# Performance work log

Measured on AMD Instinct MI355X. Metric: run time of the kernel, lower is better.

## Reference

```python
import jax, jax.numpy as jnp
import numpy as np

QMAX = 127.0  # int8 symmetric range used by quanto absmax quantizer


def setup_inputs() -> dict:
    key = jax.random.key(0)
    k1, k2, k3 = jax.random.split(key, 3)
    x = jax.random.normal(k1, (4, 2048, 1600), dtype=jnp.float32)
    weight = jax.random.normal(k2, (1600, 6400), dtype=jnp.float32) * 0.02  # Conv1D init std=0.02
    bias = jax.random.normal(k3, (6400,), dtype=jnp.float32) * 0.02
    in_scale = jnp.float32(0.02)   # calibration scale for activations
    out_scale = jnp.float32(0.05)  # calibration scale for outputs
    return {"x": x, "weight": weight, "bias": bias, "in_scale": in_scale, "out_scale": out_scale}


def reference(x, weight, bias, in_scale, out_scale):
    # --- quantize input to int8 with the fixed in_scale (QTensor.quantize) ---
    x_q = jnp.clip(jnp.round(x / in_scale), -128, 127).astype(jnp.int32)
    # --- quantize weight to int8 with absmax scale (QTensor.quantize default) ---
    w_scale = jnp.max(jnp.abs(weight)) / QMAX
    w_q = jnp.clip(jnp.round(weight / w_scale), -128, 127).astype(jnp.int32)
    # --- quantize bias to int32 at the accumulator scale ---
    bias_scale = in_scale * w_scale
    b_q = jnp.round(bias / bias_scale).astype(jnp.int32)
    # --- int32-accumulated addmm: [B*S, nx] @ [nx, nf] + [nf] ---
    bsz = x.shape[:-1]
    nx = x.shape[-1]
    acc_i32 = jnp.matmul(x_q.reshape(-1, nx), w_q,
                         preferred_element_type=jnp.int32) + b_q[None, :]
    # --- rescale int32 accumulator (scale=bias_scale) to int8 at out_scale ---
    out_q = jnp.clip(jnp.round(acc_i32.astype(jnp.float32) * (bias_scale / out_scale)),
                     -128, 127).astype(jnp.int8)
    # return the dequantized value the downstream layer would see
    out = out_q.astype(jnp.float32) * out_scale
    return out.reshape(*bsz, -1)
```

## Files before the change

kernel.cpp:

```cpp
#include <hip/hip_runtime.h>


#define M_DIM 8192
#define K_DIM 1600
#define N_DIM 6400
#define QMAXF 127.0f

typedef __attribute__((ext_vector_type(4))) int int4v;


__device__ __forceinline__ void load_lds16(const void* gptr, void* lptr) {
    __builtin_amdgcn_global_load_lds((__attribute__((address_space(1))) void*)gptr,
                                     (__attribute__((address_space(3))) void*)lptr,
                                     16, 0, 0);
}

__global__ void wmax_kernel(const float* __restrict__ w,
                            unsigned int* __restrict__ wmax_bits, int n4) {
    __shared__ float smax[4];
    const float4* w4 = (const float4*)w;
    int i = blockIdx.x * blockDim.x + threadIdx.x;
    int stride = gridDim.x * blockDim.x;
    float m = 0.0f;
    for (; i < n4; i += stride) {
        float4 v = w4[i];
        m = fmaxf(m, fmaxf(fmaxf(fabsf(v.x), fabsf(v.y)),
                           fmaxf(fabsf(v.z), fabsf(v.w))));
    }
#pragma unroll
    for (int off = 32; off > 0; off >>= 1)
        m = fmaxf(m, __shfl_down(m, off, 64));
    const int wave = threadIdx.x >> 6;
    if ((threadIdx.x & 63) == 0) smax[wave] = m;
    __syncthreads();
    if (threadIdx.x == 0) {
        float mm = fmaxf(fmaxf(smax[0], smax[1]), fmaxf(smax[2], smax[3]));
        atomicMax(wmax_bits, __float_as_uint(mm));
    }
}

__global__ void quantx_kernel(const float* __restrict__ x, signed char* __restrict__ xq,
                              const float* __restrict__ in_scale_p, int n4) {
    int i = blockIdx.x * blockDim.x + threadIdx.x;
    if (i >= n4) return;
    float s = *in_scale_p;
    float4 v = ((const float4*)x)[i];
    float a = fminf(fmaxf(rintf(v.x / s), -128.0f), 127.0f);
    float b = fminf(fmaxf(rintf(v.y / s), -128.0f), 127.0f);
    float c = fminf(fmaxf(rintf(v.z / s), -128.0f), 127.0f);
    float d = fminf(fmaxf(rintf(v.w / s), -128.0f), 127.0f);
    char4 packed = make_char4((signed char)a, (signed char)b,
                              (signed char)c, (signed char)d);
    ((char4*)xq)[i] = packed;
}

__global__ void quantw_kernel(const float* __restrict__ w, signed char* __restrict__ wT,
                              const unsigned int* __restrict__ wmax_bits) {
    __shared__ signed char tile[64 * 80];
    const float wscale = __uint_as_float(*wmax_bits) / QMAXF;
    const int n0 = blockIdx.x * 64;
    const int k0 = blockIdx.y * 64;
    const int tid = threadIdx.x;
    const int nn = tid & 63;
    const int kb = tid >> 6;
#pragma unroll
    for (int p = 0; p < 16; ++p) {
        const int kk = p * 4 + kb;
        float v = w[(size_t)(k0 + kk) * N_DIM + n0 + nn];
        float q = fminf(fmaxf(rintf(v / wscale), -128.0f), 127.0f);
        tile[nn * 80 + kk] = (signed char)q;
    }
    __syncthreads();
    const int n_loc = tid >> 2;
    const int kq = tid & 3;
    int4v val = *(const int4v*)&tile[n_loc * 80 + kq * 16];
    *(int4v*)&wT[(size_t)(n0 + n_loc) * K_DIM + k0 + kq * 16] = val;
}

__global__ __launch_bounds__(256, 2) void gemm_i8_kernel(
        const signed char* __restrict__ xq, const signed char* __restrict__ wTq,
        const float* __restrict__ bias, const unsigned int* __restrict__ wmax_bits,
        const float* __restrict__ in_scale_p, const float* __restrict__ out_scale_p,
        float* __restrict__ out) {
    __shared__ signed char A_lds[2][128 * 64];
    __shared__ signed char B_lds[2][128 * 64];

    const int tid   = threadIdx.x;
    const int wave  = tid >> 6;
    const int lane  = tid & 63;
    const int quad  = lane >> 4;
    const int l15   = lane & 15;
    const int waveM = wave >> 1;
    const int waveN = wave & 1;

    const int gid   = blockIdx.x;
    const int xcd   = gid & 7;
    const int idx   = gid >> 3;
    const int n_blk = idx >> 3;
    const int m_blk = (xcd << 3) | (idx & 7);

    const int blockN0 = n_blk * 128;
    const int blockM0 = m_blk * 128;

    const signed char* Ag = xq  + (size_t)blockM0 * K_DIM;
    const signed char* Bg = wTq + (size_t)blockN0 * K_DIM;

    const int srow = wave * 16 + (lane >> 2);
    const int scol = (((lane & 3) ^ ((lane >> 3) & 3)) * 16);

    int4v acc[4][4];
    const int4v zero4 = {0, 0, 0, 0};
#pragma unroll
    for (int i = 0; i < 4; ++i)
#pragma unroll
        for (int j = 0; j < 4; ++j) acc[i][j] = zero4;

#pragma unroll
    for (int t = 0; t < 2; ++t) {
        const int r = t * 64 + srow;
        load_lds16(Ag + (size_t)r * K_DIM + scol, &A_lds[0][(t * 64 + wave * 16) * 64]);
        load_lds16(Bg + (size_t)r * K_DIM + scol, &B_lds[0][(t * 64 + wave * 16) * 64]);
    }

    const int rchunk = (quad ^ ((l15 >> 1) & 3)) * 16;

    int buf = 0;
    for (int kn = 64; kn <= K_DIM; kn += 64) {
        __syncthreads();

        if (kn < K_DIM) {
            const int nb = buf ^ 1;
#pragma unroll
            for (int t = 0; t < 2; ++t) {
                const int r = t * 64 + srow;
                load_lds16(Ag + (size_t)r * K_DIM + kn + scol,
                           &A_lds[nb][(t * 64 + wave * 16) * 64]);
                load_lds16(Bg + (size_t)r * K_DIM + kn + scol,
                           &B_lds[nb][(t * 64 + wave * 16) * 64]);
            }
        }

        int4v a[4], b[4];
#pragma unroll
        for (int mt = 0; mt < 4; ++mt)
            a[mt] = *(const int4v*)&A_lds[buf][(waveM * 64 + mt * 16 + l15) * 64 + rchunk];
#pragma unroll
        for (int nt = 0; nt < 4; ++nt)
            b[nt] = *(const int4v*)&B_lds[buf][(waveN * 64 + nt * 16 + l15) * 64 + rchunk];

#pragma unroll
        for (int mt = 0; mt < 4; ++mt)
#pragma unroll
            for (int nt = 0; nt < 4; ++nt)
                acc[mt][nt] = __builtin_amdgcn_mfma_i32_16x16x64_i8(a[mt], b[nt],
                                                                    acc[mt][nt], 0, 0, 0);
        buf ^= 1;
    }

    const float s_in  = *in_scale_p;
    const float s_out = *out_scale_p;
    const float wscale = __uint_as_float(*wmax_bits) / QMAXF;
    const float bias_scale = s_in * wscale;
    const float ratio = bias_scale / s_out;

#pragma unroll
    for (int nt = 0; nt < 4; ++nt) {
        const int col = blockN0 + waveN * 64 + nt * 16 + l15;
        const int bq = (int)rintf(bias[col] / bias_scale);
#pragma unroll
        for (int mt = 0; mt < 4; ++mt) {
#pragma unroll
            for (int r = 0; r < 4; ++r) {
                const int row = blockM0 + waveM * 64 + mt * 16 + quad * 4 + r;
                const int av = acc[mt][nt][r] + bq;
                float f = rintf((float)av * ratio);
                f = fminf(fmaxf(f, -128.0f), 127.0f);
                out[(size_t)row * N_DIM + col] = f * s_out;
            }
        }
    }
}

extern "C" void kernel_launch(void* const* d_in, const int* in_sizes, int n_in,
                              void* d_out, int out_size, void* d_ws, size_t ws_size,
                              hipStream_t stream) {
    const float* x         = (const float*)d_in[0];
    const float* w         = (const float*)d_in[1];
    const float* bias      = (const float*)d_in[2];
    const float* in_scale  = (const float*)d_in[3];
    const float* out_scale = (const float*)d_in[4];
    float* out = (float*)d_out;

    unsigned char* ws = (unsigned char*)d_ws;
    unsigned int* wmax_bits = (unsigned int*)ws;
    signed char* xq  = (signed char*)(ws + 256);
    signed char* wTq = (signed char*)(ws + 256 + (size_t)M_DIM * K_DIM);

    hipMemsetAsync(d_ws, 0, 256, stream);

    wmax_kernel<<<320, 256, 0, stream>>>(w, wmax_bits, (K_DIM * N_DIM) / 4);

    quantx_kernel<<<(M_DIM * K_DIM / 4 + 255) / 256, 256, 0, stream>>>(
        x, xq, in_scale, M_DIM * K_DIM / 4);

    dim3 wgrid(N_DIM / 64, K_DIM / 64);
    quantw_kernel<<<wgrid, 256, 0, stream>>>(w, wTq, wmax_bits);

    gemm_i8_kernel<<<3200, 256, 0, stream>>>(xq, wTq, bias, wmax_bits,
                                             in_scale, out_scale, out);
}
```

Baseline: 434.9 us.

## Triple-buffer LDS in int8 GEMM with explicit vmcnt waits

Turns the GEMM main loop from double to triple buffering. Global-to-LDS loads run two k-tiles ahead, and fine-grained s_waitcnt vmcnt counts replace the full __syncthreads, so more load latency can overlap with MFMA work. LDS use grows from 32KB to 48KB per block, which may affect the occupancy target of 2 blocks per CU. The hand-written wait counts also depend on the exact number of outstanding loads per stage.

```diff
diff --git a/kernel.cpp b/kernel.cpp
--- a/kernel.cpp
+++ b/kernel.cpp
@@ -82,8 +82,8 @@
         const float* __restrict__ bias, const unsigned int* __restrict__ wmax_bits,
         const float* __restrict__ in_scale_p, const float* __restrict__ out_scale_p,
         float* __restrict__ out) {
-    __shared__ signed char A_lds[2][128 * 64];
-    __shared__ signed char B_lds[2][128 * 64];
+    __shared__ signed char A_lds[3][128 * 64];
+    __shared__ signed char B_lds[3][128 * 64];
 
     const int tid   = threadIdx.x;
     const int wave  = tid >> 6;
@@ -115,47 +115,65 @@
 #pragma unroll
         for (int j = 0; j < 4; ++j) acc[i][j] = zero4;
 
-#pragma unroll
-    for (int t = 0; t < 2; ++t) {
-        const int r = t * 64 + srow;
-        load_lds16(Ag + (size_t)r * K_DIM + scol, &A_lds[0][(t * 64 + wave * 16) * 64]);
-        load_lds16(Bg + (size_t)r * K_DIM + scol, &B_lds[0][(t * 64 + wave * 16) * 64]);
-    }
-
     const int rchunk = (quad ^ ((l15 >> 1) & 3)) * 16;
 
-    int buf = 0;
-    for (int kn = 64; kn <= K_DIM; kn += 64) {
-        __syncthreads();
-
-        if (kn < K_DIM) {
-            const int nb = buf ^ 1;
-#pragma unroll
-            for (int t = 0; t < 2; ++t) {
-                const int r = t * 64 + srow;
-                load_lds16(Ag + (size_t)r * K_DIM + kn + scol,
-                           &A_lds[nb][(t * 64 + wave * 16) * 64]);
-                load_lds16(Bg + (size_t)r * K_DIM + kn + scol,
-                           &B_lds[nb][(t * 64 + wave * 16) * 64]);
-            }
+    const int NT = K_DIM / 64;
+
+    auto STAGE = [&](int sb, int kt) {
+        const int kof = kt * 64;
+#pragma unroll
+        for (int t = 0; t < 2; ++t) {
+            const int r = t * 64 + srow;
+            load_lds16(Ag + (size_t)r * K_DIM + kof + scol,
+                       &A_lds[sb][(t * 64 + wave * 16) * 64]);
+            load_lds16(Bg + (size_t)r * K_DIM + kof + scol,
+                       &B_lds[sb][(t * 64 + wave * 16) * 64]);
         }
-
+    };
+
+    auto COMPUTE = [&](int cb) {
         int4v a[4], b[4];
 #pragma unroll
         for (int mt = 0; mt < 4; ++mt)
-            a[mt] = *(const int4v*)&A_lds[buf][(waveM * 64 + mt * 16 + l15) * 64 + rchunk];
+            a[mt] = *(const int4v*)&A_lds[cb][(waveM * 64 + mt * 16 + l15) * 64 + rchunk];
 #pragma unroll
         for (int nt = 0; nt < 4; ++nt)
-            b[nt] = *(const int4v*)&B_lds[buf][(waveN * 64 + nt * 16 + l15) * 64 + rchunk];
-
+            b[nt] = *(const int4v*)&B_lds[cb][(waveN * 64 + nt * 16 + l15) * 64 + rchunk];
 #pragma unroll
         for (int mt = 0; mt < 4; ++mt)
 #pragma unroll
             for (int nt = 0; nt < 4; ++nt)
                 acc[mt][nt] = __builtin_amdgcn_mfma_i32_16x16x64_i8(a[mt], b[nt],
                                                                     acc[mt][nt], 0, 0, 0);
-        buf ^= 1;
-    }
+    };
+
+    STAGE(0, 0);
+    STAGE(1, 1);
+
+    int cb = 0;
+    for (int t = 0; t < NT - 2; ++t) {
+        const int sb = (cb == 0) ? 2 : cb - 1;
+        STAGE(sb, t + 2);
+        asm volatile("s_waitcnt vmcnt(8)" ::: "memory");
+        __builtin_amdgcn_s_barrier();
+        __builtin_amdgcn_sched_barrier(0);
+        COMPUTE(cb);
+        asm volatile("s_waitcnt lgkmcnt(0)" ::: "memory");
+        __builtin_amdgcn_sched_barrier(0);
+        __builtin_amdgcn_s_barrier();
+        cb = (cb == 2) ? 0 : cb + 1;
+    }
+
+    asm volatile("s_waitcnt vmcnt(4)" ::: "memory");
+    __builtin_amdgcn_s_barrier();
+    __builtin_amdgcn_sched_barrier(0);
+    COMPUTE(cb);
+    cb = (cb == 2) ? 0 : cb + 1;
+
+    asm volatile("s_waitcnt vmcnt(0)" ::: "memory");
+    __builtin_amdgcn_s_barrier();
+    __builtin_amdgcn_sched_barrier(0);
+    COMPUTE(cb);
 
     const float s_in  = *in_scale_p;
     const float s_out = *out_scale_p;
```

After: 421.1 us. 1.03x faster.
